# Kernel tuning notes

Hardware: AMD Instinct MI355X
Metric: run time of the kernel (lower is better)

## Reference

```python
import jax, jax.numpy as jnp
import numpy as np

B, S, DIM, H, DH = 2, 2048, 1024, 16, 64
INNER = H * DH


def setup_inputs() -> dict:
    key = jax.random.key(0)
    ks = jax.random.split(key, 4)
    sd = 0.02
    return {
        "x": jax.random.normal(ks[0], (B, S, DIM), dtype=jnp.float32),
        "ln_w": jnp.ones((DIM,), jnp.float32),
        "ln_b": jnp.zeros((DIM,), jnp.float32),
        "Wq": jax.random.normal(ks[1], (DIM, INNER), jnp.float32) * sd,
        "Wkv": jax.random.normal(ks[2], (DIM, 2 * INNER), jnp.float32) * sd,
        "q_gamma": jnp.ones((H, 1, DH), jnp.float32),
        "k_gamma": jnp.ones((H, 1, DH), jnp.float32),
        "Wo": jax.random.normal(ks[3], (INNER, DIM), jnp.float32) * sd,
    }


def _rmsnorm(t, gamma, scale):
    # t: (b,h,s,d); gamma: (h,1,d)
    normed = t * jax.lax.rsqrt(jnp.mean(t * t, axis=-1, keepdims=True) + 1e-8)
    return normed * scale * gamma


def reference(x, ln_w, ln_b, Wq, Wkv, q_gamma, k_gamma, Wo):
    h, dh = q_gamma.shape[0], q_gamma.shape[-1]
    b, s, _ = x.shape
    # pre-LayerNorm (eps 1e-5, biased variance)
    mean = jnp.mean(x, axis=-1, keepdims=True)
    var = jnp.var(x, axis=-1, keepdims=True)
    xn = ln_w * (x - mean) / jnp.sqrt(var + 1e-5) + ln_b
    # projections
    q = xn @ Wq                       # (b,s,h*dh)
    k, v = jnp.split(xn @ Wkv, 2, axis=-1)
    # split heads -> (b,h,s,dh)
    to_heads = lambda t: t.reshape(b, s, h, dh).transpose(0, 2, 1, 3)
    q, k, v = to_heads(q), to_heads(k), to_heads(v)
    scale = dh ** 0.5
    q = _rmsnorm(q, q_gamma, scale)
    k = _rmsnorm(k, k_gamma, scale)
    # attention (no extra 1/sqrt(d): RMSNorm scale already applied)
    dots = jnp.einsum("bhid,bhjd->bhij", q, k)
    attn = jax.nn.softmax(dots, axis=-1)
    out = jnp.einsum("bhij,bhjd->bhid", attn, v)
    out = out.transpose(0, 2, 1, 3).reshape(b, s, h * dh)
    return out @ Wo
```

## Files before the change

### kernel.cpp

```cpp
#include <hip/hip_runtime.h>
#include <hip/hip_bf16.h>

#define DEVFN __device__ __forceinline__

typedef __attribute__((ext_vector_type(8))) short short8;
typedef __attribute__((ext_vector_type(4))) short short4v;
typedef __attribute__((ext_vector_type(4))) float f32x4;

#define MFMA(a,b,c) __builtin_amdgcn_mfma_f32_16x16x32_bf16((a),(b),(c),0,0,0)

DEVFN void gload_lds16(const __hip_bfloat16* g, __hip_bfloat16* l) {
  __builtin_amdgcn_global_load_lds((const __attribute__((address_space(1))) void*)g,
                                   (__attribute__((address_space(3))) void*)l, 16, 0, 0);
}

DEVFN float bf2f(__hip_bfloat16 h) { return __bfloat162float(h); }
DEVFN __hip_bfloat16 f2bf(float f) { return __float2bfloat16(f); }

DEVFN void store_out(float* p, float v) { *p = v; }
DEVFN void store_out(__hip_bfloat16* p, float v) { *p = f2bf(v); }

__global__ __launch_bounds__(256) void ln_split_kernel(
    const float* __restrict__ x, const float* __restrict__ lw, const float* __restrict__ lb,
    __hip_bfloat16* __restrict__ xh, __hip_bfloat16* __restrict__ xl) {
  int row = blockIdx.x, t = threadIdx.x;
  float4 v = ((const float4*)(x + (size_t)row * 1024))[t];
  float s  = v.x + v.y + v.z + v.w;
  float ss = v.x*v.x + v.y*v.y + v.z*v.z + v.w*v.w;
  #pragma unroll
  for (int m = 1; m < 64; m <<= 1) { s += __shfl_xor(s, m); ss += __shfl_xor(ss, m); }
  __shared__ float red[8];
  int wv = t >> 6;
  if ((t & 63) == 0) { red[wv] = s; red[4 + wv] = ss; }
  __syncthreads();
  s  = red[0] + red[1] + red[2] + red[3];
  ss = red[4] + red[5] + red[6] + red[7];
  float mean = s * (1.f/1024.f);
  float var  = ss * (1.f/1024.f) - mean*mean;
  float inv  = rsqrtf(var + 1e-5f);
  float4 wv4 = ((const float4*)lw)[t];
  float4 bv4 = ((const float4*)lb)[t];
  float xv[4] = {v.x, v.y, v.z, v.w};
  float wa[4] = {wv4.x, wv4.y, wv4.z, wv4.w};
  float ba[4] = {bv4.x, bv4.y, bv4.z, bv4.w};
  union { short4v s4; __hip_bfloat16 h[4]; } uh, ul;
  #pragma unroll
  for (int j = 0; j < 4; ++j) {
    float val = (xv[j] - mean) * inv * wa[j] + ba[j];
    __hip_bfloat16 hi = f2bf(val);
    uh.h[j] = hi;
    ul.h[j] = f2bf(val - bf2f(hi));
  }
  ((short4v*)(xh + (size_t)row * 1024))[t] = uh.s4;
  ((short4v*)(xl + (size_t)row * 1024))[t] = ul.s4;
}

__global__ __launch_bounds__(256) void wprep_kernel(
    const float* __restrict__ Wq, const float* __restrict__ Wkv, const float* __restrict__ Wo,
    __hip_bfloat16* __restrict__ Wqk_h, __hip_bfloat16* __restrict__ Wqk_l,
    __hip_bfloat16* __restrict__ Wv, __hip_bfloat16* __restrict__ Wot) {
  __shared__ float tile[64][68];
  int bid = blockIdx.x, t = threadIdx.x;
  const float* src; int srcN, kt, nt, drow;
  __hip_bfloat16 *dh, *dl;
  if (bid < 256) {
    src = Wq; srcN = 1024; kt = bid >> 4; nt = bid & 15;
    dh = Wqk_h; dl = Wqk_l; drow = nt * 64;
  } else if (bid < 768) {
    int r = bid - 256; src = Wkv; srcN = 2048; kt = r >> 5; nt = r & 31;
    if (nt < 16) { dh = Wqk_h; dl = Wqk_l; drow = 1024 + nt * 64; }
    else         { dh = Wv;    dl = nullptr; drow = (nt - 16) * 64; }
  } else {
    int r = bid - 768; src = Wo; srcN = 1024; kt = r >> 4; nt = r & 15;
    dh = Wot; dl = nullptr; drow = nt * 64;
  }
  int lr = t >> 2, c = t & 3;
  const float* sp = src + (size_t)(kt*64 + lr) * srcN + nt*64 + c*16;
  float* tr = &tile[lr][c*16];
  ((float4*)tr)[0] = ((const float4*)sp)[0];
  ((float4*)tr)[1] = ((const float4*)sp)[1];
  ((float4*)tr)[2] = ((const float4*)sp)[2];
  ((float4*)tr)[3] = ((const float4*)sp)[3];
  __syncthreads();
  union { short8 s8[2]; __hip_bfloat16 h[16]; } hh, ll;
  #pragma unroll
  for (int e = 0; e < 16; ++e) {
    float wv = tile[c*16 + e][lr];
    __hip_bfloat16 hi = f2bf(wv);
    hh.h[e] = hi;
    ll.h[e] = f2bf(wv - bf2f(hi));
  }
  size_t doff = (size_t)(drow + lr) * 1024 + kt*64 + c*16;
  ((short8*)(dh + doff))[0] = hh.s8[0];
  ((short8*)(dh + doff))[1] = hh.s8[1];
  if (dl) {
    ((short8*)(dl + doff))[0] = ll.s8[0];
    ((short8*)(dl + doff))[1] = ll.s8[1];
  }
}

__global__ __launch_bounds__(256) void gemm_dual_kernel(
    const __hip_bfloat16* __restrict__ Ah, const __hip_bfloat16* __restrict__ Al,
    const __hip_bfloat16* __restrict__ Bh, const __hip_bfloat16* __restrict__ Bl,
    __hip_bfloat16* __restrict__ Ch, __hip_bfloat16* __restrict__ Cl,
    const float* __restrict__ qg, const float* __restrict__ kg) {
  __shared__ __align__(16) __hip_bfloat16 sAh[128*32], sAl[128*32], sBh[128*32], sBl[128*32];
  const int K = 1024, N = 2048;
  int mt = blockIdx.x, nt = blockIdx.y;
  int t = threadIdx.x, w = t >> 6, l = t & 63;
  int wr = w >> 1, wc = w & 1, lr = l & 15, lk = (l >> 4) * 8;
  f32x4 acc[4][4] = {};
  for (int k0 = 0; k0 < K; k0 += 32) {
    #pragma unroll
    for (int i = 0; i < 2; ++i) {
      int ci = i*256 + t;
      size_t ga = (size_t)(mt*128 + (ci >> 2)) * K + k0 + (ci & 3) * 8;
      size_t gb = (size_t)(nt*128 + (ci >> 2)) * K + k0 + (ci & 3) * 8;
      int ldst = (i*256 + w*64) * 8;
      gload_lds16(Ah + ga, sAh + ldst);
      gload_lds16(Al + ga, sAl + ldst);
      gload_lds16(Bh + gb, sBh + ldst);
      gload_lds16(Bl + gb, sBl + ldst);
    }
    __syncthreads();
    short8 ah[4], al[4], bh[4], bl[4];
    #pragma unroll
    for (int m = 0; m < 4; ++m) {
      int ro = (wr*64 + m*16 + lr)*32 + lk;
      ah[m] = *(const short8*)(sAh + ro);
      al[m] = *(const short8*)(sAl + ro);
    }
    #pragma unroll
    for (int n = 0; n < 4; ++n) {
      int ro = (wc*64 + n*16 + lr)*32 + lk;
      bh[n] = *(const short8*)(sBh + ro);
      bl[n] = *(const short8*)(sBl + ro);
    }
    #pragma unroll
    for (int m = 0; m < 4; ++m)
      #pragma unroll
      for (int n = 0; n < 4; ++n) {
        acc[m][n] = MFMA(ah[m], bh[n], acc[m][n]);
        acc[m][n] = MFMA(ah[m], bl[n], acc[m][n]);
        acc[m][n] = MFMA(al[m], bh[n], acc[m][n]);
      }
    __syncthreads();
  }
  int col0 = nt*128 + wc*64;
  int head = col0 >> 6;
  const float* gamma = (head < 16) ? (qg + head*64) : (kg + (head - 16)*64);
  float g[4];
  #pragma unroll
  for (int nf = 0; nf < 4; ++nf) g[nf] = gamma[nf*16 + lr];
  #pragma unroll
  for (int m = 0; m < 4; ++m) {
    #pragma unroll
    for (int r = 0; r < 4; ++r) {
      float ss2 = 0.f;
      #pragma unroll
      for (int nf = 0; nf < 4; ++nf) ss2 += acc[m][nf][r] * acc[m][nf][r];
      #pragma unroll
      for (int msk = 1; msk < 16; msk <<= 1) ss2 += __shfl_xor(ss2, msk);
      float scl = rsqrtf(ss2 * (1.f/64.f) + 1e-8f) * 8.f;
      int row = mt*128 + wr*64 + m*16 + (l >> 4)*4 + r;
      #pragma unroll
      for (int nf = 0; nf < 4; ++nf) {
        float val = acc[m][nf][r] * scl * g[nf];
        __hip_bfloat16 hi = f2bf(val);
        size_t off = (size_t)row * N + col0 + nf*16 + lr;
        Ch[off] = hi;
        Cl[off] = f2bf(val - bf2f(hi));
      }
    }
  }
}

template <typename OUT_T>
__global__ __launch_bounds__(256) void gemm_single_kernel(
    const __hip_bfloat16* __restrict__ A, const __hip_bfloat16* __restrict__ Bt,
    OUT_T* __restrict__ C, int N) {
  __shared__ __align__(16) __hip_bfloat16 sA[128*32], sB[128*32];
  const int K = 1024;
  int mt = blockIdx.x, nt = blockIdx.y;
  int t = threadIdx.x, w = t >> 6, l = t & 63;
  int wr = w >> 1, wc = w & 1, lr = l & 15, lk = (l >> 4) * 8;
  f32x4 acc[4][4] = {};
  for (int k0 = 0; k0 < K; k0 += 32) {
    #pragma unroll
    for (int i = 0; i < 2; ++i) {
      int ci = i*256 + t;
      size_t ga = (size_t)(mt*128 + (ci >> 2)) * K + k0 + (ci & 3) * 8;
      size_t gb = (size_t)(nt*128 + (ci >> 2)) * K + k0 + (ci & 3) * 8;
      int ldst = (i*256 + w*64) * 8;
      gload_lds16(A + ga, sA + ldst);
      gload_lds16(Bt + gb, sB + ldst);
    }
    __syncthreads();
    short8 af[4], bf[4];
    #pragma unroll
    for (int m = 0; m < 4; ++m) af[m] = *(const short8*)(sA + (wr*64 + m*16 + lr)*32 + lk);
    #pragma unroll
    for (int n = 0; n < 4; ++n) bf[n] = *(const short8*)(sB + (wc*64 + n*16 + lr)*32 + lk);
    #pragma unroll
    for (int m = 0; m < 4; ++m)
      #pragma unroll
      for (int n = 0; n < 4; ++n)
        acc[m][n] = MFMA(af[m], bf[n], acc[m][n]);
    __syncthreads();
  }
  int row0 = mt*128 + wr*64, col0 = nt*128 + wc*64;
  #pragma unroll
  for (int m = 0; m < 4; ++m)
    #pragma unroll
    for (int n = 0; n < 4; ++n)
      #pragma unroll
      for (int r = 0; r < 4; ++r) {
        int row = row0 + m*16 + (l >> 4)*4 + r;
        int col = col0 + n*16 + lr;
        store_out(&C[(size_t)row * N + col], acc[m][n][r]);
      }
}

__global__ __launch_bounds__(256) void vtrans_kernel(
    const __hip_bfloat16* __restrict__ vbuf, __hip_bfloat16* __restrict__ vT) {
  __shared__ __hip_bfloat16 tile[64][72];
  int bid = blockIdx.x;
  int b = bid >> 9, h = (bid >> 5) & 15, st = bid & 31;
  int t = threadIdx.x, j = t >> 2, c = t & 3;
  const short8* src = (const short8*)(vbuf + (size_t)(b*2048 + st*64 + j) * 1024 + h*64 + c*16);
  *(short8*)&tile[j][c*16]     = src[0];
  *(short8*)&tile[j][c*16 + 8] = src[1];
  __syncthreads();
  int d = t >> 2, c2 = t & 3;
  union { short8 s8[2]; __hip_bfloat16 hh[16]; } o;
  #pragma unroll
  for (int e = 0; e < 16; ++e) o.hh[e] = tile[c2*16 + e][d];
  short8* dst = (short8*)(vT + (size_t)((b*16 + h)*64 + d) * 2048 + st*64 + c2*16);
  dst[0] = o.s8[0];
  dst[1] = o.s8[1];
}

__global__ __launch_bounds__(256) void attn_kernel(
    const __hip_bfloat16* __restrict__ qk_h, const __hip_bfloat16* __restrict__ qk_l,
    const __hip_bfloat16* __restrict__ vT, __hip_bfloat16* __restrict__ ao) {
  __shared__ __align__(16) __hip_bfloat16 sKh[64*64], sKl[64*64], sVt[64*64];
  __shared__ __align__(16) __hip_bfloat16 sP[4*16*64];
  int t = threadIdx.x, w = t >> 6, l = t & 63, lr = l & 15, hi = l >> 4, lk = hi * 8;
  int bh = blockIdx.x & 31, qt = blockIdx.x >> 5;
  int b = bh >> 4, h = bh & 15;
  const __hip_bfloat16* qbh = qk_h + (size_t)b * 2048 * 2048 + h * 64;
  const __hip_bfloat16* qbl = qk_l + (size_t)b * 2048 * 2048 + h * 64;
  const __hip_bfloat16* kbh = qbh + 1024;
  const __hip_bfloat16* kbl = qbl + 1024;
  const __hip_bfloat16* vtb = vT + (size_t)bh * 64 * 2048;
  int qrow = qt*64 + w*16 + lr;
  short8 qh0 = *(const short8*)(qbh + (size_t)qrow*2048 + lk);
  short8 qh1 = *(const short8*)(qbh + (size_t)qrow*2048 + 32 + lk);
  short8 ql0 = *(const short8*)(qbl + (size_t)qrow*2048 + lk);
  short8 ql1 = *(const short8*)(qbl + (size_t)qrow*2048 + 32 + lk);
  f32x4 o_acc[4] = {};
  float m_run[4], l_run[4];
  #pragma unroll
  for (int r = 0; r < 4; ++r) { m_run[r] = -1e30f; l_run[r] = 0.f; }

  int swl = lr & 7;
  int c0e = (hi ^ swl) << 3;
  int c1e = c0e ^ 32;
  int ci0 = t, ci1 = 256 + t;
  int r0 = ci0 >> 3, cs0 = (ci0 & 7) ^ (r0 & 7);
  int r1 = ci1 >> 3, cs1 = (ci1 & 7) ^ (r1 & 7);
  int ldb0 = (w*64) * 8, ldb1 = (256 + w*64) * 8;

  for (int kv0 = 0; kv0 < 2048; kv0 += 64) {
    gload_lds16(kbh + (size_t)(kv0 + r0)*2048 + cs0*8, sKh + ldb0);
    gload_lds16(kbh + (size_t)(kv0 + r1)*2048 + cs1*8, sKh + ldb1);
    gload_lds16(kbl + (size_t)(kv0 + r0)*2048 + cs0*8, sKl + ldb0);
    gload_lds16(kbl + (size_t)(kv0 + r1)*2048 + cs1*8, sKl + ldb1);
    gload_lds16(vtb + (size_t)r0*2048 + kv0 + cs0*8, sVt + ldb0);
    gload_lds16(vtb + (size_t)r1*2048 + kv0 + cs1*8, sVt + ldb1);
    __syncthreads();
    f32x4 s_acc[4];
    #pragma unroll
    for (int nf = 0; nf < 4; ++nf) {
      int rb = (nf*16 + lr) * 64;
      short8 kh0 = *(const short8*)(sKh + rb + c0e);
      short8 kh1 = *(const short8*)(sKh + rb + c1e);
      short8 kl0 = *(const short8*)(sKl + rb + c0e);
      short8 kl1 = *(const short8*)(sKl + rb + c1e);
      f32x4 sa = {};
      sa = MFMA(qh0, kh0, sa);
      sa = MFMA(qh1, kh1, sa);
      sa = MFMA(qh0, kl0, sa);
      sa = MFMA(qh1, kl1, sa);
      sa = MFMA(ql0, kh0, sa);
      sa = MFMA(ql1, kh1, sa);
      s_acc[nf] = sa;
    }
    #pragma unroll
    for (int r = 0; r < 4; ++r) {
      float mx = fmaxf(fmaxf(s_acc[0][r], s_acc[1][r]), fmaxf(s_acc[2][r], s_acc[3][r]));
      #pragma unroll
      for (int msk = 1; msk < 16; msk <<= 1) mx = fmaxf(mx, __shfl_xor(mx, msk));
      float mnew = fmaxf(m_run[r], mx);
      float corr = __expf(m_run[r] - mnew);
      m_run[r] = mnew;
      int prow = hi*4 + r;
      int pbase = (w << 10) + prow*64 + (swl );
      float rowsum = 0.f;
      #pragma unroll
      for (int nf = 0; nf < 4; ++nf) {
        float pv = __expf(s_acc[nf][r] - mnew);
        __hip_bfloat16 pb = f2bf(pv);
        int chunk = (nf << 1) | (lr >> 3);
        sP[pbase + ((chunk ^ (prow & 7)) << 3)] = pb;
        rowsum += bf2f(pb);
      }
      #pragma unroll
      for (int msk = 1; msk < 16; msk <<= 1) rowsum += __shfl_xor(rowsum, msk);
      l_run[r] = l_run[r] * corr + rowsum;
      #pragma unroll
      for (int df = 0; df < 4; ++df) o_acc[df][r] *= corr;
    }
    #pragma unroll
    for (int kk = 0; kk < 2; ++kk) {
      int vck = (((kk << 2) | hi) ^ swl) << 3;
      short8 pf = *(const short8*)(sP + (w << 10) + lr*64 + vck);
      #pragma unroll
      for (int df = 0; df < 4; ++df) {
        short8 vf = *(const short8*)(sVt + (df*16 + lr)*64 + vck);
        o_acc[df] = MFMA(pf, vf, o_acc[df]);
      }
    }
    __syncthreads();
  }
  size_t orow0 = (size_t)b*2048 + qt*64 + w*16 + hi*4;
  #pragma unroll
  for (int df = 0; df < 4; ++df)
    #pragma unroll
    for (int r = 0; r < 4; ++r) {
      float oval = o_acc[df][r] / l_run[r];
      ao[(orow0 + r) * 1024 + h*64 + df*16 + lr] = f2bf(oval);
    }
}

extern "C" void kernel_launch(void* const* d_in, const int* in_sizes, int n_in,
                              void* d_out, int out_size, void* d_ws, size_t ws_size,
                              hipStream_t stream) {
  const float* x   = (const float*)d_in[0];
  const float* lw  = (const float*)d_in[1];
  const float* lb  = (const float*)d_in[2];
  const float* Wq  = (const float*)d_in[3];
  const float* Wkv = (const float*)d_in[4];
  const float* qg  = (const float*)d_in[5];
  const float* kg  = (const float*)d_in[6];
  const float* Wo  = (const float*)d_in[7];
  float* out = (float*)d_out;
  char* ws = (char*)d_ws;
  const size_t MB = 1024 * 1024;
  __hip_bfloat16* xh    = (__hip_bfloat16*)(ws + 0);
  __hip_bfloat16* xl    = (__hip_bfloat16*)(ws + 8*MB);
  __hip_bfloat16* qk_h  = (__hip_bfloat16*)(ws + 16*MB);
  __hip_bfloat16* qk_l  = (__hip_bfloat16*)(ws + 32*MB);
  __hip_bfloat16* Wqk_h = (__hip_bfloat16*)(ws + 48*MB);
  __hip_bfloat16* Wqk_l = (__hip_bfloat16*)(ws + 52*MB);
  __hip_bfloat16* Wv    = (__hip_bfloat16*)(ws + 56*MB);
  __hip_bfloat16* Wot   = (__hip_bfloat16*)(ws + 58*MB);
  __hip_bfloat16* vT    = (__hip_bfloat16*)(ws + 60*MB);
  __hip_bfloat16* vbuf  = (__hip_bfloat16*)(ws + 8*MB);
  __hip_bfloat16* ao    = (__hip_bfloat16*)(ws + 0);

  ln_split_kernel<<<4096, 256, 0, stream>>>(x, lw, lb, xh, xl);
  wprep_kernel<<<1024, 256, 0, stream>>>(Wq, Wkv, Wo, Wqk_h, Wqk_l, Wv, Wot);
  gemm_dual_kernel<<<dim3(32, 16), 256, 0, stream>>>(xh, xl, Wqk_h, Wqk_l, qk_h, qk_l, qg, kg);
  gemm_single_kernel<__hip_bfloat16><<<dim3(32, 8), 256, 0, stream>>>(xh, Wv, vbuf, 1024);
  vtrans_kernel<<<1024, 256, 0, stream>>>(vbuf, vT);
  attn_kernel<<<1024, 256, 0, stream>>>(qk_h, qk_l, vT, ao);
  gemm_single_kernel<float><<<dim3(32, 8), 256, 0, stream>>>(ao, Wot, out, 1024);
}
```

Measured before the change: 335.2 us.

## Double-buffer K/V tiles in attention and compute row sums via MFMA

The attention kernel now double-buffers the K-high, K-low and V^T tiles in LDS, issuing async global-to-LDS loads for the next tile before computing the current one, with explicit vmcnt waits and raw barriers in place of __syncthreads. Row sums of P are accumulated with an extra MFMA against a ones vector instead of shuffle reductions. Rescaling of the running max is skipped while the new tile max stays within a threshold of the old one, and s_setprio wraps the MFMA phases. The goal is to hide load latency and cut VALU/shuffle work, at the cost of doubled LDS use (possibly lower occupancy) and reliance on hand-placed waitcnt and barrier ordering for correctness.

```diff
diff --git a/kernel.cpp b/kernel.cpp
--- a/kernel.cpp
+++ b/kernel.cpp
@@ -243,8 +243,8 @@
 __global__ __launch_bounds__(256) void attn_kernel(
     const __hip_bfloat16* __restrict__ qk_h, const __hip_bfloat16* __restrict__ qk_l,
     const __hip_bfloat16* __restrict__ vT, __hip_bfloat16* __restrict__ ao) {
-  __shared__ __align__(16) __hip_bfloat16 sKh[64*64], sKl[64*64], sVt[64*64];
-  __shared__ __align__(16) __hip_bfloat16 sP[4*16*64];
+  __shared__ __align__(16) __hip_bfloat16 sKh[2][4096], sKl[2][4096], sVt[2][4096];
+  __shared__ __align__(16) __hip_bfloat16 sP[4096];
   int t = threadIdx.x, w = t >> 6, l = t & 63, lr = l & 15, hi = l >> 4, lk = hi * 8;
   int bh = blockIdx.x & 31, qt = blockIdx.x >> 5;
   int b = bh >> 4, h = bh & 15;
@@ -259,9 +259,11 @@
   short8 ql0 = *(const short8*)(qbl + (size_t)qrow*2048 + lk);
   short8 ql1 = *(const short8*)(qbl + (size_t)qrow*2048 + 32 + lk);
   f32x4 o_acc[4] = {};
-  float m_run[4], l_run[4];
-  #pragma unroll
-  for (int r = 0; r < 4; ++r) { m_run[r] = -1e30f; l_run[r] = 0.f; }
+  f32x4 l_acc = {0.f, 0.f, 0.f, 0.f};
+  float m_run[4];
+  #pragma unroll
+  for (int r = 0; r < 4; ++r) m_run[r] = -1e30f;
+  const short8 ones = {0x3F80, 0x3F80, 0x3F80, 0x3F80, 0x3F80, 0x3F80, 0x3F80, 0x3F80};
 
   int swl = lr & 7;
   int c0e = (hi ^ swl) << 3;
@@ -271,22 +273,38 @@
   int r1 = ci1 >> 3, cs1 = (ci1 & 7) ^ (r1 & 7);
   int ldb0 = (w*64) * 8, ldb1 = (256 + w*64) * 8;
 
-  for (int kv0 = 0; kv0 < 2048; kv0 += 64) {
-    gload_lds16(kbh + (size_t)(kv0 + r0)*2048 + cs0*8, sKh + ldb0);
-    gload_lds16(kbh + (size_t)(kv0 + r1)*2048 + cs1*8, sKh + ldb1);
-    gload_lds16(kbl + (size_t)(kv0 + r0)*2048 + cs0*8, sKl + ldb0);
-    gload_lds16(kbl + (size_t)(kv0 + r1)*2048 + cs1*8, sKl + ldb1);
-    gload_lds16(vtb + (size_t)r0*2048 + kv0 + cs0*8, sVt + ldb0);
-    gload_lds16(vtb + (size_t)r1*2048 + kv0 + cs1*8, sVt + ldb1);
-    __syncthreads();
+#define STAGE(B, KV) do { \
+    gload_lds16(kbh + (size_t)((KV) + r0)*2048 + cs0*8, &sKh[B][0] + ldb0); \
+    gload_lds16(kbh + (size_t)((KV) + r1)*2048 + cs1*8, &sKh[B][0] + ldb1); \
+    gload_lds16(kbl + (size_t)((KV) + r0)*2048 + cs0*8, &sKl[B][0] + ldb0); \
+    gload_lds16(kbl + (size_t)((KV) + r1)*2048 + cs1*8, &sKl[B][0] + ldb1); \
+    gload_lds16(vtb + (size_t)r0*2048 + (KV) + cs0*8, &sVt[B][0] + ldb0); \
+    gload_lds16(vtb + (size_t)r1*2048 + (KV) + cs1*8, &sVt[B][0] + ldb1); \
+  } while (0)
+
+  STAGE(0, 0);
+  int buf = 0;
+  for (int tile = 0; tile < 32; ++tile) {
+    int kv0 = tile << 6;
+    if (tile < 31) {
+      STAGE(buf ^ 1, kv0 + 64);
+      asm volatile("s_waitcnt vmcnt(6)" ::: "memory");
+    } else {
+      asm volatile("s_waitcnt vmcnt(0)" ::: "memory");
+    }
+    __builtin_amdgcn_s_barrier();
+    const __hip_bfloat16* pKh = &sKh[buf][0];
+    const __hip_bfloat16* pKl = &sKl[buf][0];
+    const __hip_bfloat16* pVt = &sVt[buf][0];
     f32x4 s_acc[4];
+    __builtin_amdgcn_s_setprio(1);
     #pragma unroll
     for (int nf = 0; nf < 4; ++nf) {
       int rb = (nf*16 + lr) * 64;
-      short8 kh0 = *(const short8*)(sKh + rb + c0e);
-      short8 kh1 = *(const short8*)(sKh + rb + c1e);
-      short8 kl0 = *(const short8*)(sKl + rb + c0e);
-      short8 kl1 = *(const short8*)(sKl + rb + c1e);
+      short8 kh0 = *(const short8*)(pKh + rb + c0e);
+      short8 kh1 = *(const short8*)(pKh + rb + c1e);
+      short8 kl0 = *(const short8*)(pKl + rb + c0e);
+      short8 kl1 = *(const short8*)(pKl + rb + c1e);
       f32x4 sa = {};
       sa = MFMA(qh0, kh0, sa);
       sa = MFMA(qh1, kh1, sa);
@@ -296,49 +314,52 @@
       sa = MFMA(ql1, kh1, sa);
       s_acc[nf] = sa;
     }
+    __builtin_amdgcn_s_setprio(0);
     #pragma unroll
     for (int r = 0; r < 4; ++r) {
       float mx = fmaxf(fmaxf(s_acc[0][r], s_acc[1][r]), fmaxf(s_acc[2][r], s_acc[3][r]));
       #pragma unroll
       for (int msk = 1; msk < 16; msk <<= 1) mx = fmaxf(mx, __shfl_xor(mx, msk));
-      float mnew = fmaxf(m_run[r], mx);
-      float corr = __expf(m_run[r] - mnew);
-      m_run[r] = mnew;
+      if (!__all(mx <= m_run[r] + 8.f)) {
+        float mnew = fmaxf(m_run[r], mx);
+        float corr = __expf(m_run[r] - mnew);
+        m_run[r] = mnew;
+        #pragma unroll
+        for (int df = 0; df < 4; ++df) o_acc[df][r] *= corr;
+        l_acc[r] *= corr;
+      }
       int prow = hi*4 + r;
-      int pbase = (w << 10) + prow*64 + (swl );
-      float rowsum = 0.f;
+      int pbase = (w << 10) + prow*64 + swl;
       #pragma unroll
       for (int nf = 0; nf < 4; ++nf) {
-        float pv = __expf(s_acc[nf][r] - mnew);
-        __hip_bfloat16 pb = f2bf(pv);
+        float pv = __expf(s_acc[nf][r] - m_run[r]);
         int chunk = (nf << 1) | (lr >> 3);
-        sP[pbase + ((chunk ^ (prow & 7)) << 3)] = pb;
-        rowsum += bf2f(pb);
-      }
-      #pragma unroll
-      for (int msk = 1; msk < 16; msk <<= 1) rowsum += __shfl_xor(rowsum, msk);
-      l_run[r] = l_run[r] * corr + rowsum;
-      #pragma unroll
-      for (int df = 0; df < 4; ++df) o_acc[df][r] *= corr;
-    }
+        sP[pbase + ((chunk ^ (prow & 7)) << 3)] = f2bf(pv);
+      }
+    }
+    __builtin_amdgcn_s_setprio(1);
     #pragma unroll
     for (int kk = 0; kk < 2; ++kk) {
       int vck = (((kk << 2) | hi) ^ swl) << 3;
       short8 pf = *(const short8*)(sP + (w << 10) + lr*64 + vck);
+      l_acc = MFMA(pf, ones, l_acc);
       #pragma unroll
       for (int df = 0; df < 4; ++df) {
-        short8 vf = *(const short8*)(sVt + (df*16 + lr)*64 + vck);
+        short8 vf = *(const short8*)(pVt + (df*16 + lr)*64 + vck);
         o_acc[df] = MFMA(pf, vf, o_acc[df]);
       }
     }
-    __syncthreads();
-  }
+    __builtin_amdgcn_s_setprio(0);
+    __builtin_amdgcn_s_barrier();
+    buf ^= 1;
+  }
+#undef STAGE
   size_t orow0 = (size_t)b*2048 + qt*64 + w*16 + hi*4;
   #pragma unroll
   for (int df = 0; df < 4; ++df)
     #pragma unroll
     for (int r = 0; r < 4; ++r) {
-      float oval = o_acc[df][r] / l_run[r];
+      float oval = o_acc[df][r] / l_acc[r];
       ao[(orow0 + r) * 1024 + h*64 + df*16 + lr] = f2bf(oval);
     }
 }
```

Measured after the change: 328.3 us. 1.02x faster.
